# Kernel tuning notes

Measured on AMD Instinct MI355X. Metric: run time of the kernel, lower is better.

Reference implementation:

```python
import jax, jax.numpy as jnp
import numpy as np

B = 2          # hard-coded batch in module
NUMQ = 300     # DETR queries
NUMC = 20      # classes (gather repeat(1,1,20))
TOPK = 100
PATCH = 30     # patch_size=(30,30) -> 3*900=2700 embed
EMBED = 3 * PATCH * PATCH
IMG = 1024
DK = 384.0     # hard-coded d_k in get_attention


def _pos_encoding():
    pe = np.zeros((TOPK, EMBED), np.float32)
    pos = np.arange(TOPK, dtype=np.float32)[:, None]
    div = np.exp(np.arange(0, EMBED, 2, dtype=np.float32) * (-np.log(10000.0) / EMBED))
    pe[:, 0::2] = np.sin(pos * div)
    pe[:, 1::2] = np.cos(pos * div)
    return jnp.asarray(pe)


def _cxcywh_to_xyxy(b):
    cx, cy, w, h = b[..., 0], b[..., 1], b[..., 2], b[..., 3]
    return jnp.stack([cx - 0.5 * w, cy - 0.5 * h, cx + 0.5 * w, cy + 0.5 * h], axis=-1)


def _get_topk_boxes(logits, boxes_cxcywh):
    # sigmoid -> flatten (Q*C) -> topk -> query index -> gather xyxy boxes
    b, q, c = logits.shape
    prob = jax.nn.sigmoid(logits).reshape(b, q * c)
    _, idx = jax.lax.top_k(prob, TOPK)
    qidx = idx // c                                   # [B, TOPK]
    xyxy = _cxcywh_to_xyxy(boxes_cxcywh)              # [B, Q, 4]
    return jnp.take_along_axis(xyxy, qidx[:, :, None], axis=1)  # [B, TOPK, 4]


def _roi_patches(img, boxes_px):
    # img: [3, H, W]; boxes_px: [Q, 4] xyxy in pixels.
    # Emulates integer crop + F.interpolate(bilinear, align_corners=False) -> 30x30.
    x0 = jnp.round(boxes_px[:, 0]); y0 = jnp.round(boxes_px[:, 1])
    x1 = jnp.round(boxes_px[:, 2]); y1 = jnp.round(boxes_px[:, 3])
    w = x1 - x0; h = y1 - y0
    valid = ((w > 0) & (h > 0)).astype(img.dtype)     # zero-size boxes -> zeros
    H, W = img.shape[1], img.shape[2]
    g = jnp.arange(PATCH, dtype=img.dtype) + 0.5
    sy = jnp.clip(g[None, :] * h[:, None] / PATCH - 0.5, 0.0, jnp.maximum(h[:, None] - 1.0, 0.0))
    sx = jnp.clip(g[None, :] * w[:, None] / PATCH - 0.5, 0.0, jnp.maximum(w[:, None] - 1.0, 0.0))
    ay = y0[:, None] + sy                              # [Q, 30] absolute rows
    ax = x0[:, None] + sx                              # [Q, 30] absolute cols
    yf = jnp.floor(ay); xf = jnp.floor(ax)
    wy = (ay - yf)[:, :, None]                         # [Q, 30, 1]
    wx = (ax - xf)[:, None, :]                         # [Q, 1, 30]
    y0i = jnp.clip(yf, 0, H - 1).astype(jnp.int32); y1i = jnp.clip(yf + 1, 0, H - 1).astype(jnp.int32)
    x0i = jnp.clip(xf, 0, W - 1).astype(jnp.int32); x1i = jnp.clip(xf + 1, 0, W - 1).astype(jnp.int32)
    gat = lambda yi, xi: img[:, yi[:, :, None], xi[:, None, :]]   # [3, Q, 30, 30]
    top = gat(y0i, x0i) * (1 - wx) + gat(y0i, x1i) * wx
    bot = gat(y1i, x0i) * (1 - wx) + gat(y1i, x1i) * wx
    val = top * (1 - wy) + bot * wy                    # [3, Q, 30, 30]
    return jnp.transpose(val, (1, 0, 2, 3)) * valid[:, None, None, None]  # [Q, 3, 30, 30]


def setup_inputs() -> dict:
    key = jax.random.key(0)
    ks = jax.random.split(key, 8)
    def boxes(k):
        k1, k2 = jax.random.split(k)
        cxcy = 0.3 + 0.4 * jax.random.uniform(k1, (B, NUMQ, 2), jnp.float32)
        wh = 0.05 + 0.2 * jax.random.uniform(k2, (B, NUMQ, 2), jnp.float32)
        return jnp.concatenate([cxcy, wh], axis=-1)
    return {
        "g_samples": jax.random.normal(ks[0], (B, 3, IMG, IMG), jnp.float32),
        "a_samples": jax.random.normal(ks[1], (B, 3, IMG, IMG), jnp.float32),
        "g_logits": jax.random.normal(ks[2], (B, NUMQ, NUMC), jnp.float32),
        "a_logits": jax.random.normal(ks[3], (B, NUMQ, NUMC), jnp.float32),
        "g_boxes": boxes(ks[4]),
        "a_boxes": boxes(ks[5]),
        "W_ground": jax.random.normal(ks[6], (EMBED, EMBED), jnp.float32) / np.sqrt(EMBED),
        "W_aerial": jax.random.normal(ks[7], (EMBED, EMBED), jnp.float32) / np.sqrt(EMBED),
        "pos_enc": _pos_encoding(),
    }


def reference(g_samples, a_samples, g_logits, a_logits, g_boxes, a_boxes, W_ground, W_aerial, pos_enc):
    gb = _get_topk_boxes(g_logits, g_boxes)            # [B, TOPK, 4] normalized xyxy
    ab = _get_topk_boxes(a_logits, a_boxes)
    S = jnp.float32(IMG)                               # square images -> scale_fct == S
    gp = jax.vmap(_roi_patches)(g_samples, gb * S)     # [B, TOPK, 3, 30, 30]
    ap = jax.vmap(_roi_patches)(a_samples, ab * S)
    gp = gp.reshape(B, TOPK, 3, PATCH * PATCH)
    ap = ap.reshape(B, TOPK, 3, PATCH * PATCH)
    # faithful to the original permute(1,0,2,3).reshape(batch, seq, embed)
    tg = jnp.transpose(gp, (1, 0, 2, 3)).reshape(B, TOPK, EMBED) + pos_enc[None]
    ta = jnp.transpose(ap, (1, 0, 2, 3)).reshape(B, TOPK, EMBED) + pos_enc[None]
    gt = tg @ W_ground.T                               # torch Linear: x @ W^T
    at = ta @ W_aerial.T
    sim = jnp.einsum('bqd,bkd->bqk', gt, at) / jnp.sqrt(jnp.float32(DK))
    return jax.nn.softmax(sim, axis=1)                 # softmax over dim=1 as in code
```

## Files before the change

kernel.cpp:

```cpp
#include <hip/hip_runtime.h>
#include <math.h>

#define NTOPK 100
#define QC    6000
#define NC    20
#define EMBED 2700
#define IMGW  1024
#define XSTR  2704
#define YPLANE 1080000

typedef __attribute__((ext_vector_type(8))) short short8;
typedef __attribute__((ext_vector_type(4))) float f32x4;

__device__ inline short f32_bf16_rne(float x) {
  const unsigned u = __float_as_uint(x);
  return (short)((u + 0x7fffu + ((u >> 16) & 1u)) >> 16);
}
__device__ inline void split_hl(float x, short& h, short& l) {
  h = f32_bf16_rne(x);
  const float hf = __uint_as_float(((unsigned)(unsigned short)h) << 16);
  l = f32_bf16_rne(x - hf);
}
__device__ inline short8 zero8() {
  short8 z;
#pragma unroll
  for (int i = 0; i < 8; ++i) z[i] = 0;
  return z;
}

__global__ __launch_bounds__(256) void topk_boxes_kernel(
    const float* __restrict__ g_logits, const float* __restrict__ a_logits,
    const float* __restrict__ g_boxes,  const float* __restrict__ a_boxes,
    float* __restrict__ boxes_px ) {
  const int which = blockIdx.x >> 1;
  const int b     = blockIdx.x & 1;
  const float* logits = (which ? a_logits : g_logits) + b * QC;
  const float* boxes  = (which ? a_boxes  : g_boxes)  + b * 300 * 4;
  float* outb = boxes_px + (size_t)(which * 2 + b) * NTOPK * 4;

  __shared__ unsigned keys[QC];
  __shared__ int hist[4096];
  __shared__ int suf[257];
  __shared__ unsigned long long cand[256];
  __shared__ int s_cnt, s_bstar;

  const int tid = threadIdx.x;
  for (int i = tid; i < 4096; i += 256) hist[i] = 0;
  if (tid == 0) s_cnt = 0;
  __syncthreads();
  for (int j = tid; j < QC; j += 256) {
    const unsigned u = __float_as_uint(logits[j]);
    const unsigned k = u ^ ((u >> 31) ? 0xFFFFFFFFu : 0x80000000u);
    keys[j] = k;
    atomicAdd(&hist[k >> 20], 1);
  }
  __syncthreads();
  int cs = 0;
#pragma unroll
  for (int i = 0; i < 16; ++i) cs += hist[tid * 16 + i];
  suf[tid] = cs;
  if (tid == 0) suf[256] = 0;
  __syncthreads();
  for (int d = 1; d < 256; d <<= 1) {
    const int v = (tid + d < 256) ? suf[tid + d] : 0;
    __syncthreads();
    suf[tid] += v;
    __syncthreads();
  }
  if (suf[tid] >= NTOPK && (tid == 255 || suf[tid + 1] < NTOPK)) {
    int acc = suf[tid + 1];
    int bstar = tid * 16;
    for (int bb = tid * 16 + 15; bb >= tid * 16; --bb) {
      if (acc + hist[bb] >= NTOPK) { bstar = bb; break; }
      acc += hist[bb];
    }
    s_bstar = bstar;
  }
  __syncthreads();
  const unsigned bstar = (unsigned)s_bstar;
  for (int j = tid; j < QC; j += 256) {
    if ((keys[j] >> 20) >= bstar) {
      const int pos = atomicAdd(&s_cnt, 1);
      if (pos < 256)
        cand[pos] = (((unsigned long long)(~keys[j])) << 13) | (unsigned)j;
    }
  }
  __syncthreads();
  const int cnt = s_cnt < 256 ? s_cnt : 256;
  if (tid < cnt) {
    const unsigned long long me = cand[tid];
    int rank = 0;
    for (int j = 0; j < cnt; ++j) rank += (cand[j] < me);
    if (rank < NTOPK) {
      const int idx = (int)(me & 8191ULL);
      const int q = idx / NC;
      const float cx = boxes[q*4+0], cy = boxes[q*4+1];
      const float w  = boxes[q*4+2], h  = boxes[q*4+3];
      const float hw = __fmul_rn(0.5f, w), hh = __fmul_rn(0.5f, h);
      outb[rank*4+0] = __fmul_rn(__fsub_rn(cx, hw), 1024.0f);
      outb[rank*4+1] = __fmul_rn(__fsub_rn(cy, hh), 1024.0f);
      outb[rank*4+2] = __fmul_rn(__fadd_rn(cx, hw), 1024.0f);
      outb[rank*4+3] = __fmul_rn(__fadd_rn(cy, hh), 1024.0f);
    }
  }
}

__global__ __launch_bounds__(256) void roi_kernel(
    const float* __restrict__ g_samples, const float* __restrict__ a_samples,
    const float* __restrict__ boxes_px, const float* __restrict__ pos_enc,
    short* __restrict__ Xgh, short* __restrict__ Xgl,
    short* __restrict__ Xah, short* __restrict__ Xal) {
  const int bi = blockIdx.x;
  const int which = bi / 600;
  const int rem = bi % 600;
  const int p = rem / 3, c = rem % 3;
  const int b = p / 100, t = p % 100;
  const int u = t * 2 + b;
  const float* ic = (which ? a_samples : g_samples)
                    + ((size_t)b * 3 + c) * IMGW * IMGW;
  const float* bx = boxes_px + ((size_t)(which * 2 + b) * NTOPK + t) * 4;
  short* xh = (which ? Xah : Xgh) + (size_t)u * XSTR + c * 900;
  short* xl = (which ? Xal : Xgl) + (size_t)u * XSTR + c * 900;
  const float* pe = pos_enc + (size_t)(u % 100) * EMBED + c * 900;

  __shared__ float s_wy[30], s_wx[30];
  __shared__ int   s_y0i[30], s_y1i[30], s_x0i[30], s_x1i[30];
  __shared__ float s_valid;

  const float x0 = rintf(bx[0]), y0 = rintf(bx[1]);
  const float x1 = rintf(bx[2]), y1 = rintf(bx[3]);
  const float w = __fsub_rn(x1, x0), h = __fsub_rn(y1, y0);
  const int tid = threadIdx.x;
  if (tid == 0) s_valid = (w > 0.0f && h > 0.0f) ? 1.0f : 0.0f;
  if (tid < 30) {
    const float g  = (float)tid + 0.5f;
    float sy = __fsub_rn(__fdiv_rn(__fmul_rn(g, h), 30.0f), 0.5f);
    const float hm1 = fmaxf(__fsub_rn(h, 1.0f), 0.0f);
    sy = fminf(fmaxf(sy, 0.0f), hm1);
    const float ay = __fadd_rn(y0, sy);
    const float yf = floorf(ay);
    s_wy[tid]  = __fsub_rn(ay, yf);
    s_y0i[tid] = (int)fminf(fmaxf(yf, 0.0f), 1023.0f);
    s_y1i[tid] = (int)fminf(fmaxf(yf + 1.0f, 0.0f), 1023.0f);
  } else if (tid >= 32 && tid < 62) {
    const int i = tid - 32;
    const float g = (float)i + 0.5f;
    float sx = __fsub_rn(__fdiv_rn(__fmul_rn(g, w), 30.0f), 0.5f);
    const float wm1 = fmaxf(__fsub_rn(w, 1.0f), 0.0f);
    sx = fminf(fmaxf(sx, 0.0f), wm1);
    const float ax = __fadd_rn(x0, sx);
    const float xf = floorf(ax);
    s_wx[i]  = __fsub_rn(ax, xf);
    s_x0i[i] = (int)fminf(fmaxf(xf, 0.0f), 1023.0f);
    s_x1i[i] = (int)fminf(fmaxf(xf + 1.0f, 0.0f), 1023.0f);
  }
  __syncthreads();
  const float valid = s_valid;
  for (int pix = tid; pix < 900; pix += 256) {
    const int py = pix / 30, px = pix % 30;
    const int yi0 = s_y0i[py], yi1 = s_y1i[py], xi0 = s_x0i[px], xi1 = s_x1i[px];
    const float wy = s_wy[py], wx = s_wx[px];
    const float p00 = ic[yi0 * IMGW + xi0], p01 = ic[yi0 * IMGW + xi1];
    const float p10 = ic[yi1 * IMGW + xi0], p11 = ic[yi1 * IMGW + xi1];
    const float top = p00 * (1.0f - wx) + p01 * wx;
    const float bot = p10 * (1.0f - wx) + p11 * wx;
    const float val = top * (1.0f - wy) + bot * wy;
    const float x = val * valid + pe[pix];
    short hb, lb;
    split_hl(x, hb, lb);
    xh[pix] = hb;
    xl[pix] = lb;
  }
  if (c == 2 && tid < 4) {
    short* bh = (which ? Xah : Xgh) + (size_t)u * XSTR;
    short* bl = (which ? Xal : Xgl) + (size_t)u * XSTR;
    bh[2700 + tid] = 0;
    bl[2700 + tid] = 0;
  }
}

__global__ __launch_bounds__(256) void gemm_kernel(
    const short* __restrict__ Xgh, const short* __restrict__ Xgl,
    const short* __restrict__ Xah, const short* __restrict__ Xal,
    const float* __restrict__ Wg, const float* __restrict__ Wa,
    float* __restrict__ Ypart) {
  const int which = blockIdx.z;
  const int kc    = blockIdx.y;
  const short* Xh = which ? Xah : Xgh;
  const short* Xl = which ? Xal : Xgl;
  const float* W  = which ? Wa  : Wg;
  float* Y = Ypart + (size_t)kc * YPLANE + (size_t)which * 540000;
  const int n0 = blockIdx.x * 64;
  const int kbeg = kc * 704;
  const int ksteps = (kc < 3) ? 11 : 10;

  __shared__ short Ah[256 * 64], Al[256 * 64];
  __shared__ short Bh[64 * 64],  Bl[64 * 64];

  const int tid = threadIdx.x;
  const int lane = tid & 63, wid = tid >> 6;
  const int lr = lane & 15, lg = lane >> 4;

  f32x4 acc[4][4] = {};

  for (int t = 0; t < ksteps; ++t) {
    const int k0 = kbeg + t * 64;
#pragma unroll
    for (int it = 0; it < 8; ++it) {
      const int cid = it * 256 + tid;
      const int row = cid >> 3, s8 = cid & 7;
      const int k = k0 + s8 * 8;
      short8 hv = zero8(), lv = zero8();
      if (row < 200 && k < EMBED) {
        hv = *(const short8*)&Xh[(size_t)row * XSTR + k];
        lv = *(const short8*)&Xl[(size_t)row * XSTR + k];
      }
      const int off = (row << 6) + ((s8 ^ (row & 7)) << 3);
      *(short8*)&Ah[off] = hv;
      *(short8*)&Al[off] = lv;
    }
#pragma unroll
    for (int it = 0; it < 2; ++it) {
      const int cid = it * 256 + tid;
      const int row = cid >> 3, s8 = cid & 7;
      const int n = n0 + row;
      const int k = k0 + s8 * 8;
      float v[8];
#pragma unroll
      for (int e = 0; e < 8; ++e) v[e] = 0.0f;
      if (n < EMBED) {
        if (k + 8 <= EMBED) {
          const float4* s = (const float4*)&W[(size_t)n * EMBED + k];
          const float4 v0 = s[0], v1 = s[1];
          v[0]=v0.x; v[1]=v0.y; v[2]=v0.z; v[3]=v0.w;
          v[4]=v1.x; v[5]=v1.y; v[6]=v1.z; v[7]=v1.w;
        } else {
#pragma unroll
          for (int e = 0; e < 8; ++e)
            if (k + e < EMBED) v[e] = W[(size_t)n * EMBED + k + e];
        }
      }
      short8 hv, lv;
#pragma unroll
      for (int e = 0; e < 8; ++e) { short hh, ll; split_hl(v[e], hh, ll); hv[e] = hh; lv[e] = ll; }
      const int off = (row << 6) + ((s8 ^ (row & 7)) << 3);
      *(short8*)&Bh[off] = hv;
      *(short8*)&Bl[off] = lv;
    }
    __syncthreads();
#pragma unroll
    for (int ks = 0; ks < 2; ++ks) {
      short8 a_h[4], a_l[4], b_h[4], b_l[4];
#pragma unroll
      for (int mr = 0; mr < 4; ++mr) {
        const int row = (wid << 6) + mr * 16 + lr;
        const int off = (row << 6) + (((ks * 4 + lg) ^ (row & 7)) << 3);
        a_h[mr] = *(const short8*)&Ah[off];
        a_l[mr] = *(const short8*)&Al[off];
      }
#pragma unroll
      for (int nr = 0; nr < 4; ++nr) {
        const int row = nr * 16 + lr;
        const int off = (row << 6) + (((ks * 4 + lg) ^ (row & 7)) << 3);
        b_h[nr] = *(const short8*)&Bh[off];
        b_l[nr] = *(const short8*)&Bl[off];
      }
#pragma unroll
      for (int mr = 0; mr < 4; ++mr)
#pragma unroll
        for (int nr = 0; nr < 4; ++nr) {
          acc[mr][nr] = __builtin_amdgcn_mfma_f32_16x16x32_bf16(a_h[mr], b_h[nr], acc[mr][nr], 0, 0, 0);
          acc[mr][nr] = __builtin_amdgcn_mfma_f32_16x16x32_bf16(a_h[mr], b_l[nr], acc[mr][nr], 0, 0, 0);
          acc[mr][nr] = __builtin_amdgcn_mfma_f32_16x16x32_bf16(a_l[mr], b_h[nr], acc[mr][nr], 0, 0, 0);
        }
    }
    __syncthreads();
  }
#pragma unroll
  for (int mr = 0; mr < 4; ++mr) {
    const int row0 = (wid << 6) + mr * 16 + lg * 4;
    if (row0 >= 200) continue;
#pragma unroll
    for (int nr = 0; nr < 4; ++nr) {
      const int col = n0 + nr * 16 + lr;
      if (col < EMBED) {
#pragma unroll
        for (int r = 0; r < 4; ++r)
          if (row0 + r < 200) Y[(size_t)(row0 + r) * EMBED + col] = acc[mr][nr][r];
      }
    }
  }
}

__global__ __launch_bounds__(256) void reduce_kernel(
    const float4* __restrict__ Yp, float4* __restrict__ Gt) {
  const int i = blockIdx.x * 256 + threadIdx.x;
  if (i < 270000) {
    const float4 a = Yp[i], b = Yp[i + 270000];
    const float4 c = Yp[i + 540000], d = Yp[i + 810000];
    Gt[i] = make_float4(a.x + b.x + c.x + d.x, a.y + b.y + c.y + d.y,
                        a.z + b.z + c.z + d.z, a.w + b.w + c.w + d.w);
  }
}

#define SKC 60
__global__ __launch_bounds__(256) void sim_gemm_kernel(
    const float* __restrict__ Gt, const float* __restrict__ At,
    float* __restrict__ part) {
  const int kc = blockIdx.x;
  const int b2 = blockIdx.y;
  __shared__ float Gs[112][SKC];
  __shared__ float As[112][SKC];
  const int tid = threadIdx.x;
  for (int e = tid; e < 100 * 15; e += 256) {
    const int r = e / 15, c = e % 15;
    const size_t src = (size_t)(b2 * 100 + r) * EMBED + kc * SKC + c * 4;
    *(float4*)&Gs[r][c * 4] = *(const float4*)&Gt[src];
    *(float4*)&As[r][c * 4] = *(const float4*)&At[src];
  }
  __syncthreads();
  const int tx = tid & 15, ty = tid >> 4;
  float acc[7][7] = {};
  for (int kd = 0; kd < SKC; kd += 4) {
    float4 g[7], a[7];
#pragma unroll
    for (int jq = 0; jq < 7; ++jq) g[jq] = *(const float4*)&Gs[tx + 16 * jq][kd];
#pragma unroll
    for (int ik = 0; ik < 7; ++ik) a[ik] = *(const float4*)&As[ty + 16 * ik][kd];
#pragma unroll
    for (int ik = 0; ik < 7; ++ik)
#pragma unroll
      for (int jq = 0; jq < 7; ++jq)
        acc[ik][jq] += a[ik].x * g[jq].x + a[ik].y * g[jq].y +
                       a[ik].z * g[jq].z + a[ik].w * g[jq].w;
  }
  float* pb = part + (size_t)(kc * 2 + b2) * 10000;
#pragma unroll
  for (int ik = 0; ik < 7; ++ik) {
    const int k = ty + 16 * ik;
    if (k < 100) {
#pragma unroll
      for (int jq = 0; jq < 7; ++jq) {
        const int q = tx + 16 * jq;
        if (q < 100) pb[k * 100 + q] = acc[ik][jq];
      }
    }
  }
}

__global__ __launch_bounds__(256) void softmax_kernel(
    const float* __restrict__ part, float* __restrict__ out) {
  const int wid  = (blockIdx.x << 2) | (threadIdx.x >> 6);
  const int lane = threadIdx.x & 63;
  const int b2 = wid / 100, k = wid % 100;
  float s0 = 0.f, s1 = 0.f;
  for (int kc = 0; kc < 45; ++kc) {
    const float* p = part + ((size_t)(kc * 2 + b2) * 100 + k) * 100;
    s0 += p[lane];
    if (lane < 36) s1 += p[lane + 64];
  }
  const float scale = sqrtf(384.0f);
  const float v0 = s0 / scale;
  const float v1 = s1 / scale;
  float m = (lane < 36) ? fmaxf(v0, v1) : v0;
#pragma unroll
  for (int off = 32; off; off >>= 1) m = fmaxf(m, __shfl_down(m, off, 64));
  m = __shfl(m, 0, 64);
  const float e0 = expf(v0 - m);
  const float e1 = (lane < 36) ? expf(v1 - m) : 0.f;
  float d = e0 + e1;
#pragma unroll
  for (int off = 32; off; off >>= 1) d += __shfl_down(d, off, 64);
  d = __shfl(d, 0, 64);
  out[((size_t)b2 * 100 + lane) * 100 + k] = e0 / d;
  if (lane < 36) out[((size_t)b2 * 100 + lane + 64) * 100 + k] = e1 / d;
}

extern "C" void kernel_launch(void* const* d_in, const int* in_sizes, int n_in,
                              void* d_out, int out_size, void* d_ws, size_t ws_size,
                              hipStream_t stream) {
  const float* g_samples = (const float*)d_in[0];
  const float* a_samples = (const float*)d_in[1];
  const float* g_logits  = (const float*)d_in[2];
  const float* a_logits  = (const float*)d_in[3];
  const float* g_boxes   = (const float*)d_in[4];
  const float* a_boxes   = (const float*)d_in[5];
  const float* W_ground  = (const float*)d_in[6];
  const float* W_aerial  = (const float*)d_in[7];
  const float* pos_enc   = (const float*)d_in[8];
  float* out = (float*)d_out;
  float* ws  = (float*)d_ws;

  float* boxes_px = ws;
  short* Xgh = (short*)(ws + 2048);
  short* Xgl = (short*)(ws + 2048 + 270400);
  short* Xah = (short*)(ws + 2048 + 540800);
  short* Xal = (short*)(ws + 2048 + 811200);
  float* Ypart = ws + 1083648;
  float* Gt    = ws + 5403648;
  float* At    = Gt + 540000;
  float* part  = Ypart;

  topk_boxes_kernel<<<4, 256, 0, stream>>>(g_logits, a_logits, g_boxes, a_boxes, boxes_px);
  roi_kernel<<<1200, 256, 0, stream>>>(g_samples, a_samples, boxes_px, pos_enc,
                                       Xgh, Xgl, Xah, Xal);
  gemm_kernel<<<dim3(43, 4, 2), 256, 0, stream>>>(Xgh, Xgl, Xah, Xal,
                                                  W_ground, W_aerial, Ypart);
  reduce_kernel<<<1055, 256, 0, stream>>>((const float4*)Ypart, (float4*)Gt);
  sim_gemm_kernel<<<dim3(45, 2), 256, 0, stream>>>(Gt, At, part);
  softmax_kernel<<<50, 256, 0, stream>>>(part, out);
}
```

Before: 236.6 us.

## Load GEMM A operands from global directly, fuse split-K reduce into sim GEMM

The projection GEMM no longer stages the 256x64 activation tile (hi/lo bf16) in shared memory. Each wave now loads its A fragments straight from global memory into registers, which cuts LDS use and raises occupancy but adds redundant global/L2 reads. The separate split-K reduce kernel is removed and the four partial planes are summed while loading tiles in the similarity GEMM, saving a launch and a round trip through memory. The ROI kernel is split into two half-patch blocks per channel for more parallelism.

```diff
diff --git a/kernel.cpp b/kernel.cpp
--- a/kernel.cpp
+++ b/kernel.cpp
@@ -111,9 +111,11 @@
     short* __restrict__ Xgh, short* __restrict__ Xgl,
     short* __restrict__ Xah, short* __restrict__ Xal) {
   const int bi = blockIdx.x;
-  const int which = bi / 600;
-  const int rem = bi % 600;
-  const int p = rem / 3, c = rem % 3;
+  const int which = bi / 1200;
+  const int rem = bi % 1200;
+  const int p = rem / 6;
+  const int sub = rem % 6;
+  const int c = sub >> 1, half = sub & 1;
   const int b = p / 100, t = p % 100;
   const int u = t * 2 + b;
   const float* ic = (which ? a_samples : g_samples)
@@ -156,7 +158,8 @@
   }
   __syncthreads();
   const float valid = s_valid;
-  for (int pix = tid; pix < 900; pix += 256) {
+  const int pbeg = half * 450, pend = pbeg + 450;
+  for (int pix = pbeg + tid; pix < pend; pix += 256) {
     const int py = pix / 30, px = pix % 30;
     const int yi0 = s_y0i[py], yi1 = s_y1i[py], xi0 = s_x0i[px], xi1 = s_x1i[px];
     const float wy = s_wy[py], wx = s_wx[px];
@@ -171,7 +174,7 @@
     xh[pix] = hb;
     xl[pix] = lb;
   }
-  if (c == 2 && tid < 4) {
+  if (c == 2 && half == 1 && tid < 4) {
     short* bh = (which ? Xah : Xgh) + (size_t)u * XSTR;
     short* bl = (which ? Xal : Xgl) + (size_t)u * XSTR;
     bh[2700 + tid] = 0;
@@ -194,8 +197,7 @@
   const int kbeg = kc * 704;
   const int ksteps = (kc < 3) ? 11 : 10;
 
-  __shared__ short Ah[256 * 64], Al[256 * 64];
-  __shared__ short Bh[64 * 64],  Bl[64 * 64];
+  __shared__ short Bh[64 * 64], Bl[64 * 64];
 
   const int tid = threadIdx.x;
   const int lane = tid & 63, wid = tid >> 6;
@@ -205,20 +207,6 @@
 
   for (int t = 0; t < ksteps; ++t) {
     const int k0 = kbeg + t * 64;
-#pragma unroll
-    for (int it = 0; it < 8; ++it) {
-      const int cid = it * 256 + tid;
-      const int row = cid >> 3, s8 = cid & 7;
-      const int k = k0 + s8 * 8;
-      short8 hv = zero8(), lv = zero8();
-      if (row < 200 && k < EMBED) {
-        hv = *(const short8*)&Xh[(size_t)row * XSTR + k];
-        lv = *(const short8*)&Xl[(size_t)row * XSTR + k];
-      }
-      const int off = (row << 6) + ((s8 ^ (row & 7)) << 3);
-      *(short8*)&Ah[off] = hv;
-      *(short8*)&Al[off] = lv;
-    }
 #pragma unroll
     for (int it = 0; it < 2; ++it) {
       const int cid = it * 256 + tid;
@@ -250,73 +238,75 @@
     __syncthreads();
 #pragma unroll
     for (int ks = 0; ks < 2; ++ks) {
-      short8 a_h[4], a_l[4], b_h[4], b_l[4];
-#pragma unroll
-      for (int mr = 0; mr < 4; ++mr) {
-        const int row = (wid << 6) + mr * 16 + lr;
-        const int off = (row << 6) + (((ks * 4 + lg) ^ (row & 7)) << 3);
-        a_h[mr] = *(const short8*)&Ah[off];
-        a_l[mr] = *(const short8*)&Al[off];
-      }
-#pragma unroll
-      for (int nr = 0; nr < 4; ++nr) {
-        const int row = nr * 16 + lr;
-        const int off = (row << 6) + (((ks * 4 + lg) ^ (row & 7)) << 3);
-        b_h[nr] = *(const short8*)&Bh[off];
-        b_l[nr] = *(const short8*)&Bl[off];
-      }
-#pragma unroll
-      for (int mr = 0; mr < 4; ++mr)
-#pragma unroll
-        for (int nr = 0; nr < 4; ++nr) {
-          acc[mr][nr] = __builtin_amdgcn_mfma_f32_16x16x32_bf16(a_h[mr], b_h[nr], acc[mr][nr], 0, 0, 0);
-          acc[mr][nr] = __builtin_amdgcn_mfma_f32_16x16x32_bf16(a_h[mr], b_l[nr], acc[mr][nr], 0, 0, 0);
-          acc[mr][nr] = __builtin_amdgcn_mfma_f32_16x16x32_bf16(a_l[mr], b_h[nr], acc[mr][nr], 0, 0, 0);
+      const int kst = k0 + ks * 32 + lg * 8;
+      short8 ah[4], al[4], bh[4], bl[4];
+#pragma unroll
+      for (int nt = 0; nt < 4; ++nt) {
+        const int brow = nt * 16 + lr;
+        const int boff = (brow << 6) + (((ks * 4 + lg) ^ (brow & 7)) << 3);
+        bh[nt] = *(const short8*)&Bh[boff];
+        bl[nt] = *(const short8*)&Bl[boff];
+      }
+#pragma unroll
+      for (int j = 0; j < 4; ++j) {
+        const int row = (wid + 4 * j) * 16 + lr;
+        ah[j] = zero8();
+        al[j] = zero8();
+        if (row < 200 && kst < EMBED) {
+          const size_t off = (size_t)row * XSTR + kst;
+          ah[j] = *(const short8*)&Xh[off];
+          al[j] = *(const short8*)&Xl[off];
         }
+      }
+#pragma unroll
+      for (int j = 0; j < 4; ++j)
+#pragma unroll
+        for (int nt = 0; nt < 4; ++nt) {
+          acc[j][nt] = __builtin_amdgcn_mfma_f32_16x16x32_bf16(ah[j], bh[nt], acc[j][nt], 0, 0, 0);
+          acc[j][nt] = __builtin_amdgcn_mfma_f32_16x16x32_bf16(ah[j], bl[nt], acc[j][nt], 0, 0, 0);
+          acc[j][nt] = __builtin_amdgcn_mfma_f32_16x16x32_bf16(al[j], bh[nt], acc[j][nt], 0, 0, 0);
+        }
     }
     __syncthreads();
   }
 #pragma unroll
-  for (int mr = 0; mr < 4; ++mr) {
-    const int row0 = (wid << 6) + mr * 16 + lg * 4;
+  for (int j = 0; j < 4; ++j) {
+    const int row0 = (wid + 4 * j) * 16 + lg * 4;
     if (row0 >= 200) continue;
 #pragma unroll
-    for (int nr = 0; nr < 4; ++nr) {
-      const int col = n0 + nr * 16 + lr;
+    for (int nt = 0; nt < 4; ++nt) {
+      const int col = n0 + nt * 16 + lr;
       if (col < EMBED) {
 #pragma unroll
         for (int r = 0; r < 4; ++r)
-          if (row0 + r < 200) Y[(size_t)(row0 + r) * EMBED + col] = acc[mr][nr][r];
-      }
-    }
-  }
-}
-
-__global__ __launch_bounds__(256) void reduce_kernel(
-    const float4* __restrict__ Yp, float4* __restrict__ Gt) {
-  const int i = blockIdx.x * 256 + threadIdx.x;
-  if (i < 270000) {
-    const float4 a = Yp[i], b = Yp[i + 270000];
-    const float4 c = Yp[i + 540000], d = Yp[i + 810000];
-    Gt[i] = make_float4(a.x + b.x + c.x + d.x, a.y + b.y + c.y + d.y,
-                        a.z + b.z + c.z + d.z, a.w + b.w + c.w + d.w);
+          if (row0 + r < 200) Y[(size_t)(row0 + r) * EMBED + col] = acc[j][nt][r];
+      }
+    }
   }
 }
 
 #define SKC 60
 __global__ __launch_bounds__(256) void sim_gemm_kernel(
-    const float* __restrict__ Gt, const float* __restrict__ At,
-    float* __restrict__ part) {
-  const int kc = blockIdx.x;
-  const int b2 = blockIdx.y;
+    const float* __restrict__ Ypart, float* __restrict__ part) {
+  const int kc2 = blockIdx.x;
+  const int b2  = blockIdx.y;
   __shared__ float Gs[112][SKC];
   __shared__ float As[112][SKC];
   const int tid = threadIdx.x;
   for (int e = tid; e < 100 * 15; e += 256) {
     const int r = e / 15, c = e % 15;
-    const size_t src = (size_t)(b2 * 100 + r) * EMBED + kc * SKC + c * 4;
-    *(float4*)&Gs[r][c * 4] = *(const float4*)&Gt[src];
-    *(float4*)&As[r][c * 4] = *(const float4*)&At[src];
+    const size_t base = (size_t)(b2 * 100 + r) * EMBED + kc2 * SKC + c * 4;
+    float4 g = make_float4(0.f, 0.f, 0.f, 0.f);
+    float4 a = make_float4(0.f, 0.f, 0.f, 0.f);
+#pragma unroll
+    for (int pl = 0; pl < 4; ++pl) {
+      const float4 gv = *(const float4*)&Ypart[(size_t)pl * YPLANE + base];
+      const float4 av = *(const float4*)&Ypart[(size_t)pl * YPLANE + 540000 + base];
+      g.x += gv.x; g.y += gv.y; g.z += gv.z; g.w += gv.w;
+      a.x += av.x; a.y += av.y; a.z += av.z; a.w += av.w;
+    }
+    *(float4*)&Gs[r][c * 4] = g;
+    *(float4*)&As[r][c * 4] = a;
   }
   __syncthreads();
   const int tx = tid & 15, ty = tid >> 4;
@@ -334,7 +324,7 @@
         acc[ik][jq] += a[ik].x * g[jq].x + a[ik].y * g[jq].y +
                        a[ik].z * g[jq].z + a[ik].w * g[jq].w;
   }
-  float* pb = part + (size_t)(kc * 2 + b2) * 10000;
+  float* pb = part + (size_t)(kc2 * 2 + b2) * 10000;
 #pragma unroll
   for (int ik = 0; ik < 7; ++ik) {
     const int k = ty + 16 * ik;
@@ -397,16 +387,13 @@
   short* Xah = (short*)(ws + 2048 + 540800);
   short* Xal = (short*)(ws + 2048 + 811200);
   float* Ypart = ws + 1083648;
-  float* Gt    = ws + 5403648;
-  float* At    = Gt + 540000;
-  float* part  = Ypart;
+  float* part  = ws + 5403648;
 
   topk_boxes_kernel<<<4, 256, 0, stream>>>(g_logits, a_logits, g_boxes, a_boxes, boxes_px);
-  roi_kernel<<<1200, 256, 0, stream>>>(g_samples, a_samples, boxes_px, pos_enc,
+  roi_kernel<<<2400, 256, 0, stream>>>(g_samples, a_samples, boxes_px, pos_enc,
                                        Xgh, Xgl, Xah, Xal);
   gemm_kernel<<<dim3(43, 4, 2), 256, 0, stream>>>(Xgh, Xgl, Xah, Xal,
                                                   W_ground, W_aerial, Ypart);
-  reduce_kernel<<<1055, 256, 0, stream>>>((const float4*)Ypart, (float4*)Gt);
-  sim_gemm_kernel<<<dim3(45, 2), 256, 0, stream>>>(Gt, At, part);
+  sim_gemm_kernel<<<dim3(45, 2), 256, 0, stream>>>(Ypart, part);
   softmax_kernel<<<50, 256, 0, stream>>>(part, out);
 }
```

New measurement: 228.5 us. 3.4% less time.
